# Optimization experiments

Measured on AMD Instinct MI355X. Metric: run time of the kernel, lower is better.

Reference implementation:

```python
import jax, jax.numpy as jnp
import numpy as np

INPUT_SIZE = 512
HIDDEN_SIZE = 512
BATCH = 64
SEQ = 1024

def _xavier(key, shape):
    fan_in, fan_out = shape
    limit = float(np.sqrt(6.0 / (fan_in + fan_out)))
    return jax.random.uniform(key, shape, jnp.float32, -limit, limit)

def setup_inputs() -> dict:
    key = jax.random.key(0)
    ks = jax.random.split(key, 9)
    x = jax.random.normal(ks[0], (BATCH, SEQ, INPUT_SIZE), jnp.float32)
    # Concatenate the 4 input-hidden and 4 hidden-hidden weights (i,f,g,o order)
    W_i = jnp.concatenate([_xavier(ks[1 + j], (INPUT_SIZE, HIDDEN_SIZE)) for j in range(4)], axis=1)  # [I, 4H]
    W_h = jnp.concatenate([_xavier(ks[5 + j], (HIDDEN_SIZE, HIDDEN_SIZE)) for j in range(4)], axis=1)  # [H, 4H]
    b = jnp.zeros((4 * HIDDEN_SIZE,), jnp.float32)  # b_ii+b_hi etc. are both zero-init; combined bias
    return {"x": x, "W_i": W_i, "W_h": W_h, "b": b}

def reference(x, W_i, W_h, b):
    H = W_h.shape[0]
    B = x.shape[0]
    # Precompute all input projections in one big GEMM: [B, S, 4H]
    x_proj = jnp.einsum('bsi,ig->bsg', x, W_i) + b

    def step(carry, xp_t):
        h, c = carry
        gates = xp_t + h @ W_h  # [B, 4H]
        i_t = jax.nn.sigmoid(gates[:, 0*H:1*H])
        f_t = jax.nn.sigmoid(gates[:, 1*H:2*H])
        g_t = jnp.tanh(gates[:, 2*H:3*H])
        o_t = jax.nn.sigmoid(gates[:, 3*H:4*H])
        c = f_t * c + i_t * g_t
        h = o_t * jnp.tanh(c)
        return (h, c), None

    h0 = jnp.zeros((B, H), x.dtype)
    c0 = jnp.zeros((B, H), x.dtype)
    (h_t, c_t), _ = jax.lax.scan(step, (h0, c0), jnp.swapaxes(x_proj, 0, 1))
    return (h_t, c_t)
```

## Files before the change

kernel.cpp:

```cpp
#include <hip/hip_runtime.h>
#include <hip/hip_bf16.h>
#include <hip/hip_cooperative_groups.h>

namespace cg = cooperative_groups;

typedef unsigned short ushort_t;
typedef unsigned int uint32;
typedef __attribute__((ext_vector_type(8))) __bf16 bf16x8;
typedef __attribute__((ext_vector_type(4))) float f32x4;
typedef __attribute__((ext_vector_type(4))) unsigned int u32x4;

#define SEQ_LEN 1024
#define NWG 64
#define NTHR 256

#define XPACK_BYTES (64ull << 20)
#define WPACK_BYTES (4ull << 20)
#define HB_OFF  (XPACK_BYTES + WPACK_BYTES)
#define CNT_OFF (HB_OFF + (128ull << 10))
#define WS_NEED (CNT_OFF + (64ull << 10))

__device__ __forceinline__ ushort_t f2bf(float f) {
  unsigned u = __builtin_bit_cast(unsigned, f);
  unsigned r = (u + 0x7fffu + ((u >> 16) & 1u)) >> 16;
  return (ushort_t)r;
}
__device__ __forceinline__ float sigm(float x) {
  float e = __expf(-x);
  return __builtin_amdgcn_rcpf(1.f + e);
}
__device__ __forceinline__ float tanh_fast(float x) {
  float a = fabsf(x);
  float e = __expf(-2.f * a);
  float r = (1.f - e) * __builtin_amdgcn_rcpf(1.f + e);
  return copysignf(r, x);
}

__global__ void zero_mem_kernel(u32x4* p) {
  int i = blockIdx.x * blockDim.x + threadIdx.x;
  u32x4 z = {0u, 0u, 0u, 0u};
  p[i] = z;
}

__global__ void pack_x_kernel(const float* __restrict__ x, u32x4* __restrict__ xp) {
  unsigned u = blockIdx.x * blockDim.x + threadIdx.x;
  int hi = u & 3;
  int kk = (u >> 2) & 15;
  int t  = (u >> 6) & 1023;
  int b  = u >> 16;
  const float* src = x + (((size_t)b * SEQ_LEN + t) * 512 + (kk << 5) + (hi << 3));
  f32x4 f0 = *(const f32x4*)(src);
  f32x4 f1 = *(const f32x4*)(src + 4);
  u32x4 o;
  o[0] = f2bf(f0[0]) | ((uint32)f2bf(f0[1]) << 16);
  o[1] = f2bf(f0[2]) | ((uint32)f2bf(f0[3]) << 16);
  o[2] = f2bf(f1[0]) | ((uint32)f2bf(f1[1]) << 16);
  o[3] = f2bf(f1[2]) | ((uint32)f2bf(f1[3]) << 16);
  xp[(size_t)((t * 16 + kk) * 64 + b) * 4 + hi] = o;
}

__global__ void pack_w_kernel(const float* __restrict__ Wi, const float* __restrict__ Wh,
                              ushort_t* __restrict__ wp) {
  unsigned e = blockIdx.x * blockDim.x + threadIdx.x;
  int k = e >> 11;
  int col = e & 2047;
  float v = (k < 512) ? Wi[(size_t)k * 2048 + col] : Wh[(size_t)(k - 512) * 2048 + col];
  int wg  = (col & 511) >> 3;
  int tau = (col >> 2) & 1;
  int hcl = col & 3;
  int gate = col >> 9;
  int p = (hcl << 2) | gate;
  int kk = k >> 5;
  int hi = (k >> 3) & 3;
  int r = k & 7;
  int lane = (hi << 4) | p;
  wp[(size_t)wg * 32768 + (size_t)(((kk * 2) + tau) * 64 + lane) * 8 + r] = f2bf(v);
}

template<bool FAST>
__global__ void __launch_bounds__(NTHR, 1)
lstm_coop(const float* __restrict__ x, const float* __restrict__ Wi,
          const float* __restrict__ Wh, const float* __restrict__ bias,
          const u32x4* __restrict__ xpack, const u32x4* __restrict__ wpack,
          ushort_t* hbuf, uint32* cnt, float* out)
{
  __shared__ u32x4 lA[4096];
  const int tid  = threadIdx.x;
  const int wg   = blockIdx.x;
  const int lane = tid & 63;
  const int wv   = tid >> 6;
  const int hi2  = lane >> 4;
  const int lo   = lane & 15;
  const int b    = (wv << 4) | lo;

  if (FAST) {
    const u32x4* wsrc = wpack + (size_t)wg * 2048 * 2;
    for (int i = tid; i < 4096; i += NTHR) lA[i] = wsrc[i];
  } else {
    for (int uu = tid; uu < 4096; uu += NTHR) {
      int ln = uu & 63, tau = (uu >> 6) & 1, kk = uu >> 7;
      int uhi = ln >> 4, p = ln & 15;
      int gate = p & 3, hcl = p >> 2;
      int col = gate * 512 + (wg << 3) + tau * 4 + hcl;
      ushort_t tmp[8];
#pragma unroll
      for (int r = 0; r < 8; ++r) {
        int k = (kk << 5) + (uhi << 3) + r;
        float f = (k < 512) ? Wi[(size_t)k * 2048 + col] : Wh[(size_t)(k - 512) * 2048 + col];
        tmp[r] = f2bf(f);
      }
      u32x4 v;
      v[0] = tmp[0] | ((uint32)tmp[1] << 16);
      v[1] = tmp[2] | ((uint32)tmp[3] << 16);
      v[2] = tmp[4] | ((uint32)tmp[5] << 16);
      v[3] = tmp[6] | ((uint32)tmp[7] << 16);
      lA[uu] = v;
    }
  }
  __syncthreads();

  const int kh0 = (wg << 3) | hi2;
  const int kh1 = kh0 + 4;
  const float b00 = bias[0 * 512 + kh0], b01 = bias[1 * 512 + kh0];
  const float b02 = bias[2 * 512 + kh0], b03 = bias[3 * 512 + kh0];
  const float b10 = bias[0 * 512 + kh1], b11 = bias[1 * 512 + kh1];
  const float b12 = bias[2 * 512 + kh1], b13 = bias[3 * 512 + kh1];

  const int hoff0 = (((kh0 >> 5) * 256 + b * 4 + ((kh0 >> 3) & 3)) << 3) + (kh0 & 7);
  const int hoff1 = hoff0 + 4;

  bf16x8 whA[16], whB[16];
#pragma unroll
  for (int kk = 0; kk < 16; ++kk) {
    whA[kk] = __builtin_bit_cast(bf16x8, lA[((16 + kk) * 2 + 0) * 64 + lane]);
    whB[kk] = __builtin_bit_cast(bf16x8, lA[((16 + kk) * 2 + 1) * 64 + lane]);
  }

  float c0 = 0.f, c1 = 0.f, hn0 = 0.f, hn1 = 0.f;
  cg::grid_group grid = cg::this_grid();

  for (int t = 0; t < SEQ_LEN; ++t) {
    f32x4 ax0 = {b00, b01, b02, b03};
    f32x4 ax1 = {b10, b11, b12, b13};
    if (FAST) {
      const u32x4* xb = xpack + (size_t)t * 4096 + b * 4 + hi2;
#pragma unroll
      for (int kk = 0; kk < 16; ++kk) {
        bf16x8 xv = __builtin_bit_cast(bf16x8, xb[kk * 256]);
        bf16x8 a0 = __builtin_bit_cast(bf16x8, lA[(kk * 2 + 0) * 64 + lane]);
        bf16x8 a1 = __builtin_bit_cast(bf16x8, lA[(kk * 2 + 1) * 64 + lane]);
        ax0 = __builtin_amdgcn_mfma_f32_16x16x32_bf16(a0, xv, ax0, 0, 0, 0);
        ax1 = __builtin_amdgcn_mfma_f32_16x16x32_bf16(a1, xv, ax1, 0, 0, 0);
      }
    } else {
      const float* xr = x + ((size_t)b * SEQ_LEN + t) * 512 + (hi2 << 3);
#pragma unroll
      for (int kk = 0; kk < 16; ++kk) {
        f32x4 f0 = *(const f32x4*)(xr + (kk << 5));
        f32x4 f1 = *(const f32x4*)(xr + (kk << 5) + 4);
        u32x4 v;
        v[0] = f2bf(f0[0]) | ((uint32)f2bf(f0[1]) << 16);
        v[1] = f2bf(f0[2]) | ((uint32)f2bf(f0[3]) << 16);
        v[2] = f2bf(f1[0]) | ((uint32)f2bf(f1[1]) << 16);
        v[3] = f2bf(f1[2]) | ((uint32)f2bf(f1[3]) << 16);
        bf16x8 xv = __builtin_bit_cast(bf16x8, v);
        bf16x8 a0 = __builtin_bit_cast(bf16x8, lA[(kk * 2 + 0) * 64 + lane]);
        bf16x8 a1 = __builtin_bit_cast(bf16x8, lA[(kk * 2 + 1) * 64 + lane]);
        ax0 = __builtin_amdgcn_mfma_f32_16x16x32_bf16(a0, xv, ax0, 0, 0, 0);
        ax1 = __builtin_amdgcn_mfma_f32_16x16x32_bf16(a1, xv, ax1, 0, 0, 0);
      }
    }

    if (FAST) {
      if (t > 0) {
        if (tid == 0) {
          const uint32* ca = cnt + (size_t)(t - 1) * 16;
          uint32 v;
          while (true) {
            asm volatile("global_load_dword %0, %1, off sc0 sc1\n\ts_waitcnt vmcnt(0)"
                         : "=v"(v) : "v"(ca) : "memory");
            if (v >= (uint32)NWG) break;
            asm volatile("s_sleep 1" ::: "memory");
          }
        }
        __syncthreads();
      }
    }

    const u32x4* hr = (const u32x4*)hbuf + (size_t)(t & 1) * 4096 + b * 4 + hi2;
    u32x4 hreg[16];
    if (FAST) {
#pragma unroll
      for (int kk = 0; kk < 16; ++kk)
        asm volatile("global_load_dwordx4 %0, %1, off sc0 sc1"
                     : "=v"(hreg[kk]) : "v"(hr + kk * 256) : "memory");
      asm volatile("s_waitcnt vmcnt(0)" ::: "memory");
      __builtin_amdgcn_sched_barrier(0);
    } else {
#pragma unroll
      for (int kk = 0; kk < 16; ++kk) hreg[kk] = hr[kk * 256];
    }

    f32x4 ah0 = {0.f, 0.f, 0.f, 0.f};
    f32x4 ah1 = {0.f, 0.f, 0.f, 0.f};
#pragma unroll
    for (int kk = 0; kk < 16; ++kk) {
      bf16x8 hv = __builtin_bit_cast(bf16x8, hreg[kk]);
      ah0 = __builtin_amdgcn_mfma_f32_16x16x32_bf16(whA[kk], hv, ah0, 0, 0, 0);
      ah1 = __builtin_amdgcn_mfma_f32_16x16x32_bf16(whB[kk], hv, ah1, 0, 0, 0);
    }

    {
      float gi = ax0[0] + ah0[0], gf = ax0[1] + ah0[1];
      float gg = ax0[2] + ah0[2], go = ax0[3] + ah0[3];
      float it = sigm(gi), ft = sigm(gf), ot = sigm(go), gt = tanh_fast(gg);
      c0 = ft * c0 + it * gt;
      hn0 = ot * tanh_fast(c0);
    }
    {
      float gi = ax1[0] + ah1[0], gf = ax1[1] + ah1[1];
      float gg = ax1[2] + ah1[2], go = ax1[3] + ah1[3];
      float it = sigm(gi), ft = sigm(gf), ot = sigm(go), gt = tanh_fast(gg);
      c1 = ft * c1 + it * gt;
      hn1 = ot * tanh_fast(c1);
    }

    if (t < SEQ_LEN - 1) {
      ushort_t* hw = hbuf + (size_t)((t + 1) & 1) * 32768;
      if (FAST) {
        uint32 v0 = f2bf(hn0), v1 = f2bf(hn1);
        asm volatile("global_store_short %0, %1, off sc0 sc1"
                     :: "v"(hw + hoff0), "v"(v0) : "memory");
        asm volatile("global_store_short %0, %1, off sc0 sc1"
                     :: "v"(hw + hoff1), "v"(v1) : "memory");
        asm volatile("s_waitcnt vmcnt(0)" ::: "memory");
        __syncthreads();
        if (tid == 0) {
          uint32* ca = cnt + (size_t)t * 16;
          uint32 one = 1;
          asm volatile("global_atomic_add %0, %1, off sc1"
                       :: "v"(ca), "v"(one) : "memory");
        }
      } else {
        hw[hoff0] = f2bf(hn0);
        hw[hoff1] = f2bf(hn1);
        __threadfence();
        grid.sync();
        __threadfence();
      }
    } else if (!FAST) {
      __threadfence();
      grid.sync();
    }
  }

  out[(size_t)b * 512 + kh0] = hn0;
  out[(size_t)b * 512 + kh1] = hn1;
  out[32768 + (size_t)b * 512 + kh0] = c0;
  out[32768 + (size_t)b * 512 + kh1] = c1;
}

extern "C" void kernel_launch(void* const* d_in, const int* in_sizes, int n_in,
                              void* d_out, int out_size, void* d_ws, size_t ws_size,
                              hipStream_t stream) {
  const float* x    = (const float*)d_in[0];
  const float* Wi   = (const float*)d_in[1];
  const float* Wh   = (const float*)d_in[2];
  const float* bias = (const float*)d_in[3];
  float* out = (float*)d_out;

  bool fast = (d_ws != nullptr) && (ws_size >= WS_NEED);

  if (fast) {
    const u32x4* xpack = (const u32x4*)d_ws;
    const u32x4* wpack = (const u32x4*)((char*)d_ws + XPACK_BYTES);
    ushort_t* hbuf = (ushort_t*)((char*)d_ws + HB_OFF);
    uint32* cnt = (uint32*)((char*)d_ws + CNT_OFF);

    zero_mem_kernel<<<48, 256, 0, stream>>>((u32x4*)((char*)d_ws + HB_OFF));
    pack_x_kernel<<<16384, 256, 0, stream>>>(x, (u32x4*)d_ws);
    pack_w_kernel<<<8192, 256, 0, stream>>>(Wi, Wh, (ushort_t*)((char*)d_ws + XPACK_BYTES));

    void* args[] = {(void*)&x, (void*)&Wi, (void*)&Wh, (void*)&bias,
                    (void*)&xpack, (void*)&wpack, (void*)&hbuf, (void*)&cnt, (void*)&out};
    void (*kfn)(const float*, const float*, const float*, const float*,
                const u32x4*, const u32x4*, ushort_t*, uint32*, float*) = lstm_coop<true>;
    hipLaunchCooperativeKernel(reinterpret_cast<void*>(kfn), dim3(NWG), dim3(NTHR),
                               args, 0, stream);
  } else {
    ushort_t* hbuf = (ushort_t*)d_out;
    uint32* cnt = (uint32*)d_out;
    const u32x4* xpack = (const u32x4*)x;
    const u32x4* wpack = (const u32x4*)Wi;

    zero_mem_kernel<<<16, 256, 0, stream>>>((u32x4*)d_out);

    void* args[] = {(void*)&x, (void*)&Wi, (void*)&Wh, (void*)&bias,
                    (void*)&xpack, (void*)&wpack, (void*)&hbuf, (void*)&cnt, (void*)&out};
    void (*kfn)(const float*, const float*, const float*, const float*,
                const u32x4*, const u32x4*, ushort_t*, uint32*, float*) = lstm_coop<false>;
    hipLaunchCooperativeKernel(reinterpret_cast<void*>(kfn), dim3(NWG), dim3(NTHR),
                               args, 0, stream);
  }
}
```

Before: 3.699 ms.

## Replace per-step atomic counter barrier with per-wave epoch flags polled by all lanes

```diff
diff --git a/kernel.cpp b/kernel.cpp
--- a/kernel.cpp
+++ b/kernel.cpp
@@ -82,7 +82,7 @@
 lstm_coop(const float* __restrict__ x, const float* __restrict__ Wi,
           const float* __restrict__ Wh, const float* __restrict__ bias,
           const u32x4* __restrict__ xpack, const u32x4* __restrict__ wpack,
-          ushort_t* hbuf, uint32* cnt, float* out)
+          ushort_t* hbuf, uint32* flags, float* out)
 {
   __shared__ u32x4 lA[4096];
   const int tid  = threadIdx.x;
@@ -173,17 +173,15 @@
 
     if (FAST) {
       if (t > 0) {
-        if (tid == 0) {
-          const uint32* ca = cnt + (size_t)(t - 1) * 16;
-          uint32 v;
-          while (true) {
-            asm volatile("global_load_dword %0, %1, off sc0 sc1\n\ts_waitcnt vmcnt(0)"
-                         : "=v"(v) : "v"(ca) : "memory");
-            if (v >= (uint32)NWG) break;
-            asm volatile("s_sleep 1" ::: "memory");
-          }
+        const u32x4* fa = (const u32x4*)flags + lane;
+        const uint32 tt = (uint32)t;
+        while (true) {
+          u32x4 v;
+          asm volatile("global_load_dwordx4 %0, %1, off sc0 sc1\n\ts_waitcnt vmcnt(0)"
+                       : "=v"(v) : "v"(fa) : "memory");
+          bool ok = (v[0] >= tt) & (v[1] >= tt) & (v[2] >= tt) & (v[3] >= tt);
+          if (__all(ok)) break;
         }
-        __syncthreads();
       }
     }
 
@@ -234,12 +232,12 @@
         asm volatile("global_store_short %0, %1, off sc0 sc1"
                      :: "v"(hw + hoff1), "v"(v1) : "memory");
         asm volatile("s_waitcnt vmcnt(0)" ::: "memory");
-        __syncthreads();
-        if (tid == 0) {
-          uint32* ca = cnt + (size_t)t * 16;
-          uint32 one = 1;
-          asm volatile("global_atomic_add %0, %1, off sc1"
-                       :: "v"(ca), "v"(one) : "memory");
+        __builtin_amdgcn_sched_barrier(0);
+        if (lane == 0) {
+          uint32* fp = flags + (wg << 2) + wv;
+          uint32 val = (uint32)(t + 1);
+          asm volatile("global_store_dword %0, %1, off sc0 sc1"
+                       :: "v"(fp), "v"(val) : "memory");
         }
       } else {
         hw[hoff0] = f2bf(hn0);
@@ -275,28 +273,28 @@
     const u32x4* xpack = (const u32x4*)d_ws;
     const u32x4* wpack = (const u32x4*)((char*)d_ws + XPACK_BYTES);
     ushort_t* hbuf = (ushort_t*)((char*)d_ws + HB_OFF);
-    uint32* cnt = (uint32*)((char*)d_ws + CNT_OFF);
+    uint32* flags = (uint32*)((char*)d_ws + CNT_OFF);
 
     zero_mem_kernel<<<48, 256, 0, stream>>>((u32x4*)((char*)d_ws + HB_OFF));
     pack_x_kernel<<<16384, 256, 0, stream>>>(x, (u32x4*)d_ws);
     pack_w_kernel<<<8192, 256, 0, stream>>>(Wi, Wh, (ushort_t*)((char*)d_ws + XPACK_BYTES));
 
     void* args[] = {(void*)&x, (void*)&Wi, (void*)&Wh, (void*)&bias,
-                    (void*)&xpack, (void*)&wpack, (void*)&hbuf, (void*)&cnt, (void*)&out};
+                    (void*)&xpack, (void*)&wpack, (void*)&hbuf, (void*)&flags, (void*)&out};
     void (*kfn)(const float*, const float*, const float*, const float*,
                 const u32x4*, const u32x4*, ushort_t*, uint32*, float*) = lstm_coop<true>;
     hipLaunchCooperativeKernel(reinterpret_cast<void*>(kfn), dim3(NWG), dim3(NTHR),
                                args, 0, stream);
   } else {
     ushort_t* hbuf = (ushort_t*)d_out;
-    uint32* cnt = (uint32*)d_out;
+    uint32* flags = (uint32*)d_out;
     const u32x4* xpack = (const u32x4*)x;
     const u32x4* wpack = (const u32x4*)Wi;
 
     zero_mem_kernel<<<16, 256, 0, stream>>>((u32x4*)d_out);
 
     void* args[] = {(void*)&x, (void*)&Wi, (void*)&Wh, (void*)&bias,
-                    (void*)&xpack, (void*)&wpack, (void*)&hbuf, (void*)&cnt, (void*)&out};
+                    (void*)&xpack, (void*)&wpack, (void*)&hbuf, (void*)&flags, (void*)&out};
     void (*kfn)(const float*, const float*, const float*, const float*,
                 const u32x4*, const u32x4*, ushort_t*, uint32*, float*) = lstm_coop<false>;
     hipLaunchCooperativeKernel(reinterpret_cast<void*>(kfn), dim3(NWG), dim3(NTHR),
```

Result: faster. 3.231 ms (-12.7%).
